# Optimization experiments

Hardware: AMD Instinct MI355X
Metric: run time of the kernel (lower is better)

## Reference

```python
import jax, jax.numpy as jnp
import numpy as np

B, T, V, E, H, L = 64, 512, 50000, 256, 256, 9


def _lstm_dir(x, w_ih, w_hh, b, reverse):
    # x: [B,T,I]; w_ih: [4H,I]; w_hh: [4H,H]; b: [4H]. PyTorch gate order i,f,g,o.
    Bm, Hm = x.shape[0], w_hh.shape[1]
    gx = jnp.einsum('bti,gi->btg', x, w_ih) + b  # [B,T,4H] precomputed input proj

    def step(carry, g_t):
        h, c = carry
        gates = g_t + h @ w_hh.T
        i, f, g, o = jnp.split(gates, 4, axis=-1)
        c = jax.nn.sigmoid(f) * c + jax.nn.sigmoid(i) * jnp.tanh(g)
        h = jax.nn.sigmoid(o) * jnp.tanh(c)
        return (h, c), h

    init = (jnp.zeros((Bm, Hm), x.dtype), jnp.zeros((Bm, Hm), x.dtype))
    _, hs = jax.lax.scan(step, init, jnp.swapaxes(gx, 0, 1), reverse=reverse)
    return jnp.swapaxes(hs, 0, 1)  # [B,T,H]


def _bilstm_layer(x, w_ih, w_hh, b):
    fwd = _lstm_dir(x, w_ih[0], w_hh[0], b[0], False)
    bwd = _lstm_dir(x, w_ih[1], w_hh[1], b[1], True)
    return jnp.concatenate([fwd, bwd], axis=-1)  # [B,T,2H]


def _crf_nll(emissions, labels, mask, trans, start_trans, end_trans):
    # emissions: [B,T,L]; labels: [B,T] int; mask: [B,T] (mask[:,0] assumed 1)
    maskf = mask.astype(emissions.dtype)
    # gold path score
    em_lab = jnp.take_along_axis(emissions, labels[..., None], axis=2)[..., 0]  # [B,T]
    trans_sc = trans[labels[:, :-1], labels[:, 1:]]  # [B,T-1]
    score = start_trans[labels[:, 0]] + em_lab[:, 0] \
        + jnp.sum((trans_sc + em_lab[:, 1:]) * maskf[:, 1:], axis=1)
    last_idx = jnp.sum(mask, axis=1).astype(jnp.int32) - 1
    last_lab = jnp.take_along_axis(labels, last_idx[:, None].astype(labels.dtype), axis=1)[:, 0]
    score = score + end_trans[last_lab]
    # log-partition via forward algorithm (scan over time)
    alpha0 = start_trans[None, :] + emissions[:, 0]  # [B,L]

    def step(alpha, xs):
        em_t, m_t = xs
        new = jax.nn.logsumexp(alpha[:, :, None] + trans[None], axis=1) + em_t
        alpha = jnp.where(m_t[:, None] > 0, new, alpha)
        return alpha, None

    alpha, _ = jax.lax.scan(
        step, alpha0,
        (jnp.swapaxes(emissions[:, 1:], 0, 1), jnp.swapaxes(mask[:, 1:], 0, 1)))
    logZ = jax.nn.logsumexp(alpha + end_trans[None, :], axis=1)  # [B]
    return -(score - logZ).mean()


def setup_inputs() -> dict:
    key = jax.random.key(0)
    ks = jax.random.split(key, 16)
    s = 0.05
    inp = {
        'input_ids': jax.random.randint(ks[0], (B, T), 0, V),
        'attention_mask': jnp.ones((B, T), jnp.int32),
        'labels': jax.random.randint(ks[1], (B, T), 0, L),
        'emb': jax.random.normal(ks[2], (V, E), jnp.float32) * s,
        # layer 0: input size E; layer 1: input size 2H. [dir, 4H, in]
        'w_ih0': jax.random.normal(ks[3], (2, 4 * H, E), jnp.float32) * s,
        'w_hh0': jax.random.normal(ks[4], (2, 4 * H, H), jnp.float32) * s,
        'b0': jax.random.normal(ks[5], (2, 4 * H), jnp.float32) * s,
        'w_ih1': jax.random.normal(ks[6], (2, 4 * H, 2 * H), jnp.float32) * s,
        'w_hh1': jax.random.normal(ks[7], (2, 4 * H, H), jnp.float32) * s,
        'b1': jax.random.normal(ks[8], (2, 4 * H), jnp.float32) * s,
        'lin_w': jax.random.normal(ks[9], (L, 2 * H), jnp.float32) * s,
        'lin_b': jax.random.normal(ks[10], (L,), jnp.float32) * s,
        'trans': jax.random.normal(ks[11], (L, L), jnp.float32) * 0.1,
        'start_trans': jax.random.normal(ks[12], (L,), jnp.float32) * 0.1,
        'end_trans': jax.random.normal(ks[13], (L,), jnp.float32) * 0.1,
    }
    return inp


def reference(input_ids, attention_mask, labels, emb, w_ih0, w_hh0, b0,
              w_ih1, w_hh1, b1, lin_w, lin_b, trans, start_trans, end_trans):
    x = emb[input_ids]                       # [B,T,E]
    x = _bilstm_layer(x, w_ih0, w_hh0, b0)   # [B,T,2H]
    x = _bilstm_layer(x, w_ih1, w_hh1, b1)   # [B,T,2H]
    emissions = x @ lin_w.T + lin_b          # [B,T,L]
    loss = _crf_nll(emissions, labels, attention_mask, trans, start_trans, end_trans)
    return loss
```

## Files before the change

### kernel.cpp

```cpp
#include <hip/hip_runtime.h>
#include <stdint.h>
#include <stddef.h>

#define B_ 64
#define T_ 512
#define E_ 256
#define H_ 256
#define L_ 9
#define BT (B_*T_)
#define G4 1024
#define N2 2048

typedef short    bf16x8  __attribute__((ext_vector_type(8)));
typedef float    f32x4   __attribute__((ext_vector_type(4)));
typedef int      i32x4   __attribute__((ext_vector_type(4)));
typedef int      i32x8   __attribute__((ext_vector_type(8)));

__device__ __forceinline__ unsigned short f2bf(float x){
    unsigned u = __builtin_bit_cast(unsigned, x);
    u += 0x7fffu + ((u >> 16) & 1u);
    return (unsigned short)(u >> 16);
}
__device__ __forceinline__ float bf2f(unsigned short h){
    unsigned u = ((unsigned)h) << 16;
    return __builtin_bit_cast(float, u);
}

__device__ __forceinline__ unsigned char f32_e4m3(float x){
    unsigned b = __builtin_bit_cast(unsigned, x);
    unsigned s = b >> 31;
    float a = fabsf(x);
    if (a >= 448.f) return (unsigned char)((s<<7) | 0x7E);
    int E = (int)((b>>23)&255) - 127;
    if (E < -6) E = -6;
    int qi = (int)rintf(a * exp2f((float)(3 - E)));
    if (qi >= 16){ qi >>= 1; ++E; }
    if (qi == 0) return (unsigned char)(s<<7);
    unsigned mag = (qi >= 8) ? ((((unsigned)(E + 7)) << 3) | (unsigned)(qi - 8))
                             : (unsigned)qi;
    return (unsigned char)((s<<7) | mag);
}

__device__ __forceinline__ float sigm(float x){
    return __builtin_amdgcn_rcpf(1.f + __expf(-x));
}
__device__ __forceinline__ float tanh_(float x){
    float e = __expf(2.f*x);
    return 1.f - 2.f*__builtin_amdgcn_rcpf(e + 1.f);
}

__device__ __forceinline__ void lds_load16(void* lds, const void* g){
    __builtin_amdgcn_global_load_lds(
        (const __attribute__((address_space(1))) void*)g,
        (__attribute__((address_space(3))) void*)lds, 16, 0, 0);
}

__device__ __forceinline__ void barrier_lds(){
    asm volatile("s_waitcnt lgkmcnt(0)" ::: "memory");
    __builtin_amdgcn_s_barrier();
    __builtin_amdgcn_sched_barrier(0);
}

__device__ __forceinline__ void store_out(unsigned short* p, float v){ *p = f2bf(v); }
__device__ __forceinline__ void store_out(float* p, float v){ *p = v; }

__global__ void k_embed(const int* __restrict__ ids, const float* __restrict__ emb,
                        unsigned char* __restrict__ x0){
    int bt = blockIdx.x;
    int e  = threadIdx.x;
    int id = ids[bt];
    x0[(size_t)bt*E_ + e] = f32_e4m3(emb[(size_t)id*E_ + e]);
}

__global__ void k_pack_wih(const float* __restrict__ in, unsigned char* __restrict__ out, int K){
    int p = blockIdx.y;
    int k = blockIdx.x*256 + threadIdx.x;
    int dirc = p >> 10, pp = p & 1023;
    int wv = pp >> 7, rem = pp & 127;
    int uh = (rem >> 6) & 1, g = (rem >> 4) & 3, ulx = rem & 15;
    int orig = dirc*1024 + g*256 + wv*32 + uh*16 + ulx;
    out[(size_t)p*K + k] = f32_e4m3(in[(size_t)orig*K + k]);
}

__global__ void k_pack_bias(const float* __restrict__ b, float* __restrict__ bp){
    int p = blockIdx.x*256 + threadIdx.x;
    int dirc = p >> 10, pp = p & 1023;
    int wv = pp >> 7, rem = pp & 127;
    int uh = (rem >> 6) & 1, g = (rem >> 4) & 3, ulx = rem & 15;
    int orig = dirc*1024 + g*256 + wv*32 + uh*16 + ulx;
    bp[p] = b[orig];
}

__global__ void k_pack_wfp8(const float* __restrict__ whh, unsigned char* __restrict__ wpk){
    int idx = blockIdx.x*256 + threadIdx.x;
    int lane = idx & 63;
    int uh   = (idx >> 6) & 1;
    int g    = (idx >> 7) & 3;
    int kt   = (idx >> 9) & 1;
    int wv   = (idx >> 10) & 7;
    int dir  = (idx >> 13) & 1;
    int ulx = lane & 15, hi4 = lane >> 4;
    int row = g*256 + wv*32 + uh*16 + ulx;
    int k0 = kt*128 + hi4*32;
    const float* src = whh + ((size_t)dir*G4 + row)*H_ + k0;
    unsigned char* dst = wpk + (size_t)idx*32;
    #pragma unroll
    for (int q = 0; q < 32; ++q) dst[q] = f32_e4m3(src[q]);
}

__global__ __launch_bounds__(256) void k_gemm_fp8(const unsigned char* __restrict__ A,
                                                  const unsigned char* __restrict__ Bm,
                                                  const float* __restrict__ bias,
                                                  unsigned short* __restrict__ C,
                                                  int M, int N, int K){
    __shared__ __align__(16) unsigned char As[16384];
    __shared__ __align__(16) unsigned char Bs[16384];
    int tid = threadIdx.x, lane = tid & 63, w = tid >> 6;
    int wm = w >> 1, wn = w & 1;
    int tileM = blockIdx.y * 128, tileN = blockIdx.x * 128;
    f32x4 acc[4][4] = {};
    for (int k0 = 0; k0 < K; k0 += 128){
        #pragma unroll
        for (int p = 0; p < 4; ++p){
            int idx = (p*256 + tid)*16;
            int ks = idx >> 12, rem = idx & 4095, row = rem >> 5;
            int jsrc = (rem & 16) ^ ((row & 4) << 2);
            lds_load16((char*)As + idx, A + (size_t)(tileM + row)*K + k0 + ks*32 + jsrc);
            lds_load16((char*)Bs + idx, Bm + (size_t)(tileN + row)*K + k0 + ks*32 + jsrc);
        }
        __syncthreads();
        int ks = lane >> 4, m15 = lane & 15;
        i32x8 af[4], bfv[4];
        #pragma unroll
        for (int mf = 0; mf < 4; ++mf){
            int r = wm*64 + mf*16 + m15;
            int base = ks*4096 + r*32, sw = (r & 4) << 2;
            i32x4 lo = *(const i32x4*)((const char*)As + base + sw);
            i32x4 hi = *(const i32x4*)((const char*)As + base + (16 ^ sw));
            af[mf] = __builtin_shufflevector(lo, hi, 0,1,2,3,4,5,6,7);
        }
        #pragma unroll
        for (int nf = 0; nf < 4; ++nf){
            int r = wn*64 + nf*16 + m15;
            int base = ks*4096 + r*32, sw = (r & 4) << 2;
            i32x4 lo = *(const i32x4*)((const char*)Bs + base + sw);
            i32x4 hi = *(const i32x4*)((const char*)Bs + base + (16 ^ sw));
            bfv[nf] = __builtin_shufflevector(lo, hi, 0,1,2,3,4,5,6,7);
        }
        #pragma unroll
        for (int mf = 0; mf < 4; ++mf)
            #pragma unroll
            for (int nf = 0; nf < 4; ++nf)
                acc[mf][nf] = __builtin_amdgcn_mfma_scale_f32_16x16x128_f8f6f4(
                                  af[mf], bfv[nf], acc[mf][nf],
                                  0, 0, 0, 0x7f7f7f7f, 0, 0x7f7f7f7f);
        barrier_lds();
    }
    #pragma unroll
    for (int mf = 0; mf < 4; ++mf){
        #pragma unroll
        for (int nf = 0; nf < 4; ++nf){
            int row0 = tileM + wm*64 + mf*16 + (lane >> 4)*4;
            int col  = tileN + wn*64 + nf*16 + (lane & 15);
            float bv = bias[col];
            #pragma unroll
            for (int r = 0; r < 4; ++r)
                C[(size_t)(row0 + r)*N + col] = f2bf(acc[mf][nf][r] + bv);
        }
    }
}

template<typename OutT>
__global__ __launch_bounds__(512, 2)
void k_rec_mfma(const unsigned short* __restrict__ gx,
                const unsigned char* __restrict__ wpk,
                OutT* __restrict__ out){
    int blk = blockIdx.x;
    int dir = blk & 1, bg = blk >> 1;
    int tid = threadIdx.x, lane = tid & 63, w = tid >> 6;
    int ul = lane & 15, hi4 = lane >> 4;
    int batch = bg*4 + hi4;

    __shared__ __align__(16) unsigned char hlds[2][32][16][8];
    {
        unsigned long long* hz = (unsigned long long*)hlds;
        for (int i = tid; i < 1024; i += 512) hz[i] = 0ull;
    }

    i32x8 wf[2][4][2];
    {
        const i32x8* wb = (const i32x8*)wpk;
        #pragma unroll
        for (int kt = 0; kt < 2; ++kt)
            #pragma unroll
            for (int g = 0; g < 4; ++g)
                #pragma unroll
                for (int uh = 0; uh < 2; ++uh)
                    wf[kt][g][uh] = wb[((((size_t)(dir*8 + w)*2 + kt)*4 + g)*2 + uh)*64 + lane];
    }
    __syncthreads();

    const unsigned short* gp = gx + (size_t)(batch*T_ + (dir ? T_-1 : 0))*N2
                                  + dir*1024 + w*128 + ul;
    ptrdiff_t dstep = dir ? -(ptrdiff_t)N2 : (ptrdiff_t)N2;

    unsigned short gxr[8];
    #pragma unroll
    for (int uh = 0; uh < 2; ++uh)
        #pragma unroll
        for (int g = 0; g < 4; ++g)
            gxr[uh*4+g] = gp[uh*64 + g*16];

    float c0 = 0.f, c1 = 0.f;
    int u0 = w*32 + ul, u1 = u0 + 16;
    OutT* ob = out + (size_t)batch*T_*512 + dir*256;

    for (int s = 0; s < T_; ++s){
        int buf = s & 1;
        f32x4 acc[4][2];
        #pragma unroll
        for (int g = 0; g < 4; ++g)
            #pragma unroll
            for (int uh = 0; uh < 2; ++uh)
                acc[g][uh] = (f32x4){ bf2f(gxr[uh*4+g]), 0.f, 0.f, 0.f };

        gp += dstep;
        unsigned short gxn[8];
        #pragma unroll
        for (int uh = 0; uh < 2; ++uh)
            #pragma unroll
            for (int g = 0; g < 4; ++g)
                gxn[uh*4+g] = gp[uh*64 + g*16];

        const unsigned long long* hrow = (const unsigned long long*)&hlds[buf][0][0][0];
        #pragma unroll
        for (int kt = 0; kt < 2; ++kt){
            unsigned long long a0 = hrow[(kt*16 + hi4*4 + 0)*16 + ul];
            unsigned long long a1 = hrow[(kt*16 + hi4*4 + 1)*16 + ul];
            unsigned long long a2 = hrow[(kt*16 + hi4*4 + 2)*16 + ul];
            unsigned long long a3 = hrow[(kt*16 + hi4*4 + 3)*16 + ul];
            i32x8 af = (i32x8){ (int)a0, (int)(a0>>32), (int)a1, (int)(a1>>32),
                                (int)a2, (int)(a2>>32), (int)a3, (int)(a3>>32) };
            #pragma unroll
            for (int g = 0; g < 4; ++g)
                #pragma unroll
                for (int uh = 0; uh < 2; ++uh)
                    acc[g][uh] = __builtin_amdgcn_mfma_scale_f32_16x16x128_f8f6f4(
                                     af, wf[kt][g][uh], acc[g][uh],
                                     0, 0, 0, 0x7f7f7f7f, 0, 0x7f7f7f7f);
        }

        int tt = dir ? (T_-1-s) : s;
        float h0, h1;
        {
            float xi = acc[0][0][0], xf = acc[1][0][0], xg = acc[2][0][0], xo = acc[3][0][0];
            c0 = sigm(xf)*c0 + sigm(xi)*tanh_(xg);
            h0 = sigm(xo)*tanh_(c0);
        }
        {
            float xi = acc[0][1][0], xf = acc[1][1][0], xg = acc[2][1][0], xo = acc[3][1][0];
            c1 = sigm(xf)*c1 + sigm(xi)*tanh_(xg);
            h1 = sigm(xo)*tanh_(c1);
        }

        unsigned char hb0, hb1;
#if __has_builtin(__builtin_amdgcn_cvt_pk_fp8_f32)
        {
            int pk = __builtin_amdgcn_cvt_pk_fp8_f32(h0, h1, 0, false);
            hb0 = (unsigned char)(pk & 0xff);
            hb1 = (unsigned char)((pk >> 8) & 0xff);
        }
#else
        hb0 = f32_e4m3(h0); hb1 = f32_e4m3(h1);
#endif
        hlds[buf^1][u0>>3][hi4*4][u0&7] = hb0;
        hlds[buf^1][u1>>3][hi4*4][u1&7] = hb1;

        if constexpr (sizeof(OutT) == 1){
            ((unsigned char*)ob)[(size_t)tt*512 + u0] = hb0;
            ((unsigned char*)ob)[(size_t)tt*512 + u1] = hb1;
        } else {
            store_out(&ob[(size_t)tt*512 + u0], h0);
            store_out(&ob[(size_t)tt*512 + u1], h1);
        }

        #pragma unroll
        for (int i = 0; i < 8; ++i) gxr[i] = gxn[i];
        barrier_lds();
    }
}

__global__ __launch_bounds__(256) void k_linear(const float* __restrict__ x,
                                                const float* __restrict__ w,
                                                const float* __restrict__ bias,
                                                float* __restrict__ em){
    int wv = threadIdx.x >> 6, lane = threadIdx.x & 63;
    int bt = blockIdx.x*4 + wv;
    const float4* xp = (const float4*)(x + (size_t)bt*(2*H_) + lane*8);
    float4 xa = xp[0], xb = xp[1];
    #pragma unroll
    for (int l = 0; l < L_; ++l){
        const float4* wp = (const float4*)(w + (size_t)l*(2*H_) + lane*8);
        float4 wa = wp[0], wb = wp[1];
        float p = xa.x*wa.x + xa.y*wa.y + xa.z*wa.z + xa.w*wa.w
                + xb.x*wb.x + xb.y*wb.y + xb.z*wb.z + xb.w*wb.w;
        #pragma unroll
        for (int o = 32; o; o >>= 1) p += __shfl_xor(p, o);
        if (lane == 0) em[(size_t)bt*L_ + l] = p + bias[l];
    }
}

__global__ void k_crf(const float* __restrict__ em, const int* __restrict__ labels,
                      const int* __restrict__ mask, const float* __restrict__ trans,
                      const float* __restrict__ st, const float* __restrict__ et,
                      float* __restrict__ out){
    int b = blockIdx.x, lane = threadIdx.x;
    __shared__ float tr[L_*L_];
    for (int i = lane; i < L_*L_; i += 64) tr[i] = trans[i];
    __syncthreads();
    const float* e  = em + (size_t)b*T_*L_;
    const int* lab  = labels + b*T_;
    const int* mk   = mask + b*T_;
    float sc = 0.f; int msum = 0;
    for (int t = lane; t < T_; t += 64){
        msum += mk[t];
        if (t >= 1)
            sc += (tr[lab[t-1]*L_ + lab[t]] + e[t*L_ + lab[t]]) * (float)mk[t];
    }
    #pragma unroll
    for (int o = 32; o; o >>= 1){ sc += __shfl_xor(sc, o); msum += __shfl_xor(msum, o); }
    int lj = lane < L_ ? lane : 0;
    float alpha = (lane < L_) ? (st[lj] + e[lj]) : -3.0e38f;
    for (int t = 1; t < T_; ++t){
        float v[L_]; float m = -3.0e38f;
        #pragma unroll
        for (int i = 0; i < L_; ++i){
            float ai = __shfl(alpha, i);
            v[i] = ai + tr[i*L_ + lj];
            m = fmaxf(m, v[i]);
        }
        float ssum = 0.f;
        #pragma unroll
        for (int i = 0; i < L_; ++i) ssum += __expf(v[i] - m);
        float nw = m + __logf(ssum) + e[t*L_ + lj];
        if (lane < L_ && mk[t] > 0) alpha = nw;
    }
    float av = (lane < L_) ? alpha + et[lj] : -3.0e38f;
    float m2 = av;
    #pragma unroll
    for (int o = 32; o; o >>= 1) m2 = fmaxf(m2, __shfl_xor(m2, o));
    float s2 = (lane < L_) ? __expf(av - m2) : 0.f;
    #pragma unroll
    for (int o = 32; o; o >>= 1) s2 += __shfl_xor(s2, o);
    if (lane == 0){
        float logZ = m2 + __logf(s2);
        int last = msum - 1;
        float score = sc + st[lab[0]] + e[lab[0]] + et[lab[last]];
        atomicAdd(out, (logZ - score) * (1.f/(float)B_));
    }
}

extern "C" void kernel_launch(void* const* d_in, const int* in_sizes, int n_in,
                              void* d_out, int out_size, void* d_ws, size_t ws_size,
                              hipStream_t stream){
    (void)in_sizes; (void)n_in; (void)out_size; (void)ws_size;
    const int*   ids    = (const int*)d_in[0];
    const int*   amask  = (const int*)d_in[1];
    const int*   labels = (const int*)d_in[2];
    const float* emb    = (const float*)d_in[3];
    const float* w_ih0  = (const float*)d_in[4];
    const float* w_hh0  = (const float*)d_in[5];
    const float* b0     = (const float*)d_in[6];
    const float* w_ih1  = (const float*)d_in[7];
    const float* w_hh1  = (const float*)d_in[8];
    const float* b1     = (const float*)d_in[9];
    const float* lin_w  = (const float*)d_in[10];
    const float* lin_b  = (const float*)d_in[11];
    const float* trans  = (const float*)d_in[12];
    const float* st     = (const float*)d_in[13];
    const float* et     = (const float*)d_in[14];
    float* out = (float*)d_out;

    char* ws = (char*)d_ws;
    size_t o = 0;
    auto alloc = [&](size_t bytes)->char*{
        char* p = ws + o; o = (o + bytes + 255) & ~(size_t)255; return p;
    };
    unsigned char*  x0    = (unsigned char*)alloc((size_t)BT*E_);
    unsigned char*  wih0p = (unsigned char*)alloc((size_t)N2*E_);
    unsigned char*  wih1p = (unsigned char*)alloc((size_t)N2*512);
    unsigned char*  wpk0  = (unsigned char*)alloc(16384*32);
    unsigned char*  wpk1  = (unsigned char*)alloc(16384*32);
    float*          bp0   = (float*)alloc(N2*4);
    float*          bp1   = (float*)alloc(N2*4);
    unsigned short* gx    = (unsigned short*)alloc((size_t)BT*N2*2);
    unsigned char*  xc1   = (unsigned char*)alloc((size_t)BT*512);
    float*          xc2   = (float*)alloc((size_t)BT*512*4);
    float*          em    = (float*)alloc((size_t)BT*L_*4 + 1024);

    hipMemsetAsync(d_out, 0, sizeof(float), stream);

    k_pack_wih<<<dim3(E_/256, N2), 256, 0, stream>>>(w_ih0, wih0p, E_);
    k_pack_wih<<<dim3(512/256, N2), 256, 0, stream>>>(w_ih1, wih1p, 512);
    k_pack_bias<<<N2/256, 256, 0, stream>>>(b0, bp0);
    k_pack_bias<<<N2/256, 256, 0, stream>>>(b1, bp1);
    k_pack_wfp8<<<16384/256, 256, 0, stream>>>(w_hh0, wpk0);
    k_pack_wfp8<<<16384/256, 256, 0, stream>>>(w_hh1, wpk1);
    k_embed<<<BT, E_, 0, stream>>>(ids, emb, x0);

    k_gemm_fp8<<<dim3(N2/128, BT/128), 256, 0, stream>>>(x0, wih0p, bp0, gx, BT, N2, E_);
    k_rec_mfma<unsigned char><<<32, 512, 0, stream>>>(gx, wpk0, xc1);
    k_gemm_fp8<<<dim3(N2/128, BT/128), 256, 0, stream>>>(xc1, wih1p, bp1, gx, BT, N2, 512);
    k_rec_mfma<float><<<32, 512, 0, stream>>>(gx, wpk1, xc2);

    k_linear<<<BT/4, 256, 0, stream>>>(xc2, lin_w, lin_b, em);
    k_crf<<<B_, 64, 0, stream>>>(em, labels, amask, trans, st, et, out);
}
```

Before: 1.317 ms.

## Double-buffer GEMM, vectorize recurrence gate loads, split MFMA chains, bf16 second-layer output

```diff
diff --git a/kernel.cpp b/kernel.cpp
--- a/kernel.cpp
+++ b/kernel.cpp
@@ -15,6 +15,7 @@
 typedef float    f32x4   __attribute__((ext_vector_type(4)));
 typedef int      i32x4   __attribute__((ext_vector_type(4)));
 typedef int      i32x8   __attribute__((ext_vector_type(8)));
+typedef unsigned short u16x8 __attribute__((ext_vector_type(8)));
 
 __device__ __forceinline__ unsigned short f2bf(float x){
     unsigned u = __builtin_bit_cast(unsigned, x);
@@ -49,6 +50,14 @@
     return 1.f - 2.f*__builtin_amdgcn_rcpf(e + 1.f);
 }
 
+__device__ __forceinline__ unsigned char f32_fp8(float x){
+#if __has_builtin(__builtin_amdgcn_cvt_pk_fp8_f32)
+    return (unsigned char)(__builtin_amdgcn_cvt_pk_fp8_f32(x, x, 0, false) & 0xff);
+#else
+    return f32_e4m3(x);
+#endif
+}
+
 __device__ __forceinline__ void lds_load16(void* lds, const void* g){
     __builtin_amdgcn_global_load_lds(
         (const __attribute__((address_space(1))) void*)g,
@@ -60,9 +69,6 @@
     __builtin_amdgcn_s_barrier();
     __builtin_amdgcn_sched_barrier(0);
 }
-
-__device__ __forceinline__ void store_out(unsigned short* p, float v){ *p = f2bf(v); }
-__device__ __forceinline__ void store_out(float* p, float v){ *p = v; }
 
 __global__ void k_embed(const int* __restrict__ ids, const float* __restrict__ emb,
                         unsigned char* __restrict__ x0){
@@ -77,7 +83,7 @@
     int k = blockIdx.x*256 + threadIdx.x;
     int dirc = p >> 10, pp = p & 1023;
     int wv = pp >> 7, rem = pp & 127;
-    int uh = (rem >> 6) & 1, g = (rem >> 4) & 3, ulx = rem & 15;
+    int ulx = rem >> 3, uh = (rem >> 2) & 1, g = rem & 3;
     int orig = dirc*1024 + g*256 + wv*32 + uh*16 + ulx;
     out[(size_t)p*K + k] = f32_e4m3(in[(size_t)orig*K + k]);
 }
@@ -86,7 +92,7 @@
     int p = blockIdx.x*256 + threadIdx.x;
     int dirc = p >> 10, pp = p & 1023;
     int wv = pp >> 7, rem = pp & 127;
-    int uh = (rem >> 6) & 1, g = (rem >> 4) & 3, ulx = rem & 15;
+    int ulx = rem >> 3, uh = (rem >> 2) & 1, g = rem & 3;
     int orig = dirc*1024 + g*256 + wv*32 + uh*16 + ulx;
     bp[p] = b[orig];
 }
@@ -113,38 +119,48 @@
                                                   const float* __restrict__ bias,
                                                   unsigned short* __restrict__ C,
                                                   int M, int N, int K){
-    __shared__ __align__(16) unsigned char As[16384];
-    __shared__ __align__(16) unsigned char Bs[16384];
+    __shared__ __align__(16) unsigned char As[2][16384];
+    __shared__ __align__(16) unsigned char Bs[2][16384];
     int tid = threadIdx.x, lane = tid & 63, w = tid >> 6;
     int wm = w >> 1, wn = w & 1;
-    int tileM = blockIdx.y * 128, tileN = blockIdx.x * 128;
-    f32x4 acc[4][4] = {};
-    for (int k0 = 0; k0 < K; k0 += 128){
+    int nwg = gridDim.x, qch = nwg >> 3;
+    int nid = (blockIdx.x & 7)*qch + (blockIdx.x >> 3);
+    int tileM = (nid >> 4) * 128, tileN = (nid & 15) * 128;
+    int nC = K >> 7;
+
+    auto stage = [&](int c, int buf){
         #pragma unroll
         for (int p = 0; p < 4; ++p){
             int idx = (p*256 + tid)*16;
             int ks = idx >> 12, rem = idx & 4095, row = rem >> 5;
             int jsrc = (rem & 16) ^ ((row & 4) << 2);
-            lds_load16((char*)As + idx, A + (size_t)(tileM + row)*K + k0 + ks*32 + jsrc);
-            lds_load16((char*)Bs + idx, Bm + (size_t)(tileN + row)*K + k0 + ks*32 + jsrc);
+            lds_load16(&As[buf][idx], A + (size_t)(tileM + row)*K + c*128 + ks*32 + jsrc);
+            lds_load16(&Bs[buf][idx], Bm + (size_t)(tileN + row)*K + c*128 + ks*32 + jsrc);
         }
-        __syncthreads();
+    };
+
+    stage(0, 0);
+    __syncthreads();
+    f32x4 acc[4][4] = {};
+    for (int c = 0; c < nC; ++c){
+        int buf = c & 1;
+        if (c + 1 < nC) stage(c + 1, buf ^ 1);
         int ks = lane >> 4, m15 = lane & 15;
         i32x8 af[4], bfv[4];
         #pragma unroll
         for (int mf = 0; mf < 4; ++mf){
             int r = wm*64 + mf*16 + m15;
             int base = ks*4096 + r*32, sw = (r & 4) << 2;
-            i32x4 lo = *(const i32x4*)((const char*)As + base + sw);
-            i32x4 hi = *(const i32x4*)((const char*)As + base + (16 ^ sw));
+            i32x4 lo = *(const i32x4*)(&As[buf][base + sw]);
+            i32x4 hi = *(const i32x4*)(&As[buf][base + (16 ^ sw)]);
             af[mf] = __builtin_shufflevector(lo, hi, 0,1,2,3,4,5,6,7);
         }
         #pragma unroll
         for (int nf = 0; nf < 4; ++nf){
             int r = wn*64 + nf*16 + m15;
             int base = ks*4096 + r*32, sw = (r & 4) << 2;
-            i32x4 lo = *(const i32x4*)((const char*)Bs + base + sw);
-            i32x4 hi = *(const i32x4*)((const char*)Bs + base + (16 ^ sw));
+            i32x4 lo = *(const i32x4*)(&Bs[buf][base + sw]);
+            i32x4 hi = *(const i32x4*)(&Bs[buf][base + (16 ^ sw)]);
             bfv[nf] = __builtin_shufflevector(lo, hi, 0,1,2,3,4,5,6,7);
         }
         #pragma unroll
@@ -154,7 +170,7 @@
                 acc[mf][nf] = __builtin_amdgcn_mfma_scale_f32_16x16x128_f8f6f4(
                                   af[mf], bfv[nf], acc[mf][nf],
                                   0, 0, 0, 0x7f7f7f7f, 0, 0x7f7f7f7f);
-        barrier_lds();
+        __syncthreads();
     }
     #pragma unroll
     for (int mf = 0; mf < 4; ++mf){
@@ -201,109 +217,112 @@
     __syncthreads();
 
     const unsigned short* gp = gx + (size_t)(batch*T_ + (dir ? T_-1 : 0))*N2
-                                  + dir*1024 + w*128 + ul;
+                                  + dir*1024 + w*128 + ul*8;
     ptrdiff_t dstep = dir ? -(ptrdiff_t)N2 : (ptrdiff_t)N2;
 
-    unsigned short gxr[8];
-    #pragma unroll
-    for (int uh = 0; uh < 2; ++uh)
-        #pragma unroll
-        for (int g = 0; g < 4; ++g)
-            gxr[uh*4+g] = gp[uh*64 + g*16];
-
+    u16x8 gxr = *(const u16x8*)gp;
     float c0 = 0.f, c1 = 0.f;
     int u0 = w*32 + ul, u1 = u0 + 16;
     OutT* ob = out + (size_t)batch*T_*512 + dir*256;
 
-    for (int s = 0; s < T_; ++s){
-        int buf = s & 1;
-        f32x4 acc[4][2];
-        #pragma unroll
-        for (int g = 0; g < 4; ++g)
-            #pragma unroll
-            for (int uh = 0; uh < 2; ++uh)
-                acc[g][uh] = (f32x4){ bf2f(gxr[uh*4+g]), 0.f, 0.f, 0.f };
-
-        gp += dstep;
-        unsigned short gxn[8];
-        #pragma unroll
-        for (int uh = 0; uh < 2; ++uh)
-            #pragma unroll
-            for (int g = 0; g < 4; ++g)
-                gxn[uh*4+g] = gp[uh*64 + g*16];
-
-        const unsigned long long* hrow = (const unsigned long long*)&hlds[buf][0][0][0];
-        #pragma unroll
-        for (int kt = 0; kt < 2; ++kt){
-            unsigned long long a0 = hrow[(kt*16 + hi4*4 + 0)*16 + ul];
-            unsigned long long a1 = hrow[(kt*16 + hi4*4 + 1)*16 + ul];
-            unsigned long long a2 = hrow[(kt*16 + hi4*4 + 2)*16 + ul];
-            unsigned long long a3 = hrow[(kt*16 + hi4*4 + 3)*16 + ul];
-            i32x8 af = (i32x8){ (int)a0, (int)(a0>>32), (int)a1, (int)(a1>>32),
-                                (int)a2, (int)(a2>>32), (int)a3, (int)(a3>>32) };
-            #pragma unroll
-            for (int g = 0; g < 4; ++g)
-                #pragma unroll
-                for (int uh = 0; uh < 2; ++uh)
-                    acc[g][uh] = __builtin_amdgcn_mfma_scale_f32_16x16x128_f8f6f4(
-                                     af, wf[kt][g][uh], acc[g][uh],
-                                     0, 0, 0, 0x7f7f7f7f, 0, 0x7f7f7f7f);
-        }
-
-        int tt = dir ? (T_-1-s) : s;
-        float h0, h1;
-        {
-            float xi = acc[0][0][0], xf = acc[1][0][0], xg = acc[2][0][0], xo = acc[3][0][0];
-            c0 = sigm(xf)*c0 + sigm(xi)*tanh_(xg);
-            h0 = sigm(xo)*tanh_(c0);
-        }
-        {
-            float xi = acc[0][1][0], xf = acc[1][1][0], xg = acc[2][1][0], xo = acc[3][1][0];
-            c1 = sigm(xf)*c1 + sigm(xi)*tanh_(xg);
-            h1 = sigm(xo)*tanh_(c1);
-        }
-
-        unsigned char hb0, hb1;
-#if __has_builtin(__builtin_amdgcn_cvt_pk_fp8_f32)
-        {
-            int pk = __builtin_amdgcn_cvt_pk_fp8_f32(h0, h1, 0, false);
-            hb0 = (unsigned char)(pk & 0xff);
-            hb1 = (unsigned char)((pk >> 8) & 0xff);
-        }
-#else
-        hb0 = f32_e4m3(h0); hb1 = f32_e4m3(h1);
-#endif
-        hlds[buf^1][u0>>3][hi4*4][u0&7] = hb0;
-        hlds[buf^1][u1>>3][hi4*4][u1&7] = hb1;
-
-        if constexpr (sizeof(OutT) == 1){
-            ((unsigned char*)ob)[(size_t)tt*512 + u0] = hb0;
-            ((unsigned char*)ob)[(size_t)tt*512 + u1] = hb1;
-        } else {
-            store_out(&ob[(size_t)tt*512 + u0], h0);
-            store_out(&ob[(size_t)tt*512 + u1], h1);
-        }
-
-        #pragma unroll
-        for (int i = 0; i < 8; ++i) gxr[i] = gxn[i];
-        barrier_lds();
-    }
-}
-
-__global__ __launch_bounds__(256) void k_linear(const float* __restrict__ x,
+#define REC_STEP(SV, BUF)                                                          \
+    {                                                                              \
+        const unsigned long long* hrow = (const unsigned long long*)&hlds[BUF][0][0][0]; \
+        unsigned long long a00 = hrow[(hi4*4 + 0)*16 + ul];                        \
+        unsigned long long a01 = hrow[(hi4*4 + 1)*16 + ul];                        \
+        unsigned long long a02 = hrow[(hi4*4 + 2)*16 + ul];                        \
+        unsigned long long a03 = hrow[(hi4*4 + 3)*16 + ul];                        \
+        unsigned long long a10 = hrow[(16 + hi4*4 + 0)*16 + ul];                   \
+        unsigned long long a11 = hrow[(16 + hi4*4 + 1)*16 + ul];                   \
+        unsigned long long a12 = hrow[(16 + hi4*4 + 2)*16 + ul];                   \
+        unsigned long long a13 = hrow[(16 + hi4*4 + 3)*16 + ul];                   \
+        i32x8 af0 = (i32x8){ (int)a00, (int)(a00>>32), (int)a01, (int)(a01>>32),   \
+                             (int)a02, (int)(a02>>32), (int)a03, (int)(a03>>32) }; \
+        i32x8 af1 = (i32x8){ (int)a10, (int)(a10>>32), (int)a11, (int)(a11>>32),   \
+                             (int)a12, (int)(a12>>32), (int)a13, (int)(a13>>32) }; \
+        gp += dstep;                                                               \
+        u16x8 gxn = *(const u16x8*)gp;                                             \
+        f32x4 acc0[4], acc1[4];                                                    \
+        _Pragma("unroll")                                                          \
+        for (int g = 0; g < 4; ++g){                                               \
+            acc0[g] = (f32x4){ bf2f(gxr[g]),   0.f, 0.f, 0.f };                    \
+            acc1[g] = (f32x4){ bf2f(gxr[4+g]), 0.f, 0.f, 0.f };                    \
+        }                                                                          \
+                                                          \
+        __builtin_amdgcn_s_setprio(1);                                             \
+        _Pragma("unroll")                                                          \
+        for (int g = 0; g < 4; ++g)                                                \
+            acc0[g] = __builtin_amdgcn_mfma_scale_f32_16x16x128_f8f6f4(            \
+                          af0, wf[0][g][0], acc0[g], 0, 0, 0, 0x7f7f7f7f, 0, 0x7f7f7f7f); \
+        _Pragma("unroll")                                                          \
+        for (int g = 0; g < 4; ++g)                                                \
+            acc0[g] = __builtin_amdgcn_mfma_scale_f32_16x16x128_f8f6f4(            \
+                          af1, wf[1][g][0], acc0[g], 0, 0, 0, 0x7f7f7f7f, 0, 0x7f7f7f7f); \
+        __builtin_amdgcn_s_setprio(0);                                             \
+                                           \
+        float h0;                                                                  \
+        {                                                                          \
+            float xi = acc0[0][0], xf = acc0[1][0], xg = acc0[2][0], xo = acc0[3][0]; \
+            c0 = sigm(xf)*c0 + sigm(xi)*tanh_(xg);                                 \
+            h0 = sigm(xo)*tanh_(c0);                                               \
+        }                                                                          \
+        unsigned char hb0 = f32_fp8(h0);                                           \
+        hlds[BUF^1][u0>>3][hi4*4][u0&7] = hb0;                                     \
+                                                          \
+        __builtin_amdgcn_s_setprio(1);                                             \
+        _Pragma("unroll")                                                          \
+        for (int g = 0; g < 4; ++g)                                                \
+            acc1[g] = __builtin_amdgcn_mfma_scale_f32_16x16x128_f8f6f4(            \
+                          af0, wf[0][g][1], acc1[g], 0, 0, 0, 0x7f7f7f7f, 0, 0x7f7f7f7f); \
+        _Pragma("unroll")                                                          \
+        for (int g = 0; g < 4; ++g)                                                \
+            acc1[g] = __builtin_amdgcn_mfma_scale_f32_16x16x128_f8f6f4(            \
+                          af1, wf[1][g][1], acc1[g], 0, 0, 0, 0x7f7f7f7f, 0, 0x7f7f7f7f); \
+        __builtin_amdgcn_s_setprio(0);                                             \
+        float h1;                                                                  \
+        {                                                                          \
+            float xi = acc1[0][0], xf = acc1[1][0], xg = acc1[2][0], xo = acc1[3][0]; \
+            c1 = sigm(xf)*c1 + sigm(xi)*tanh_(xg);                                 \
+            h1 = sigm(xo)*tanh_(c1);                                               \
+        }                                                                          \
+        unsigned char hb1 = f32_fp8(h1);                                           \
+        hlds[BUF^1][u1>>3][hi4*4][u1&7] = hb1;                                     \
+        barrier_lds();                                                             \
+                       \
+        int tt = dir ? (T_-1-(SV)) : (SV);                                         \
+        if constexpr (sizeof(OutT) == 1){                                          \
+            ((unsigned char*)ob)[(size_t)tt*512 + u0] = hb0;                       \
+            ((unsigned char*)ob)[(size_t)tt*512 + u1] = hb1;                       \
+        } else {                                                                   \
+            ob[(size_t)tt*512 + u0] = (OutT)f2bf(h0);                              \
+            ob[(size_t)tt*512 + u1] = (OutT)f2bf(h1);                              \
+        }                                                                          \
+        gxr = gxn;                                                                 \
+    }
+
+    for (int s = 0; s < T_; s += 2){
+        REC_STEP(s, 0)
+        REC_STEP(s+1, 1)
+    }
+#undef REC_STEP
+}
+
+__global__ __launch_bounds__(256) void k_linear(const unsigned short* __restrict__ x,
                                                 const float* __restrict__ w,
                                                 const float* __restrict__ bias,
                                                 float* __restrict__ em){
     int wv = threadIdx.x >> 6, lane = threadIdx.x & 63;
     int bt = blockIdx.x*4 + wv;
-    const float4* xp = (const float4*)(x + (size_t)bt*(2*H_) + lane*8);
-    float4 xa = xp[0], xb = xp[1];
+    u16x8 xv = *(const u16x8*)(x + (size_t)bt*(2*H_) + lane*8);
+    float xf[8];
+    #pragma unroll
+    for (int j = 0; j < 8; ++j) xf[j] = bf2f(xv[j]);
     #pragma unroll
     for (int l = 0; l < L_; ++l){
         const float4* wp = (const float4*)(w + (size_t)l*(2*H_) + lane*8);
         float4 wa = wp[0], wb = wp[1];
-        float p = xa.x*wa.x + xa.y*wa.y + xa.z*wa.z + xa.w*wa.w
-                + xb.x*wb.x + xb.y*wb.y + xb.z*wb.z + xb.w*wb.w;
+        float p = xf[0]*wa.x + xf[1]*wa.y + xf[2]*wa.z + xf[3]*wa.w
+                + xf[4]*wb.x + xf[5]*wb.y + xf[6]*wb.z + xf[7]*wb.w;
         #pragma unroll
         for (int o = 32; o; o >>= 1) p += __shfl_xor(p, o);
         if (lane == 0) em[(size_t)bt*L_ + l] = p + bias[l];
@@ -395,7 +414,7 @@
     float*          bp1   = (float*)alloc(N2*4);
     unsigned short* gx    = (unsigned short*)alloc((size_t)BT*N2*2);
     unsigned char*  xc1   = (unsigned char*)alloc((size_t)BT*512);
-    float*          xc2   = (float*)alloc((size_t)BT*512*4);
+    unsigned short* xc2   = (unsigned short*)alloc((size_t)BT*512*2);
     float*          em    = (float*)alloc((size_t)BT*L_*4 + 1024);
 
     hipMemsetAsync(d_out, 0, sizeof(float), stream);
@@ -408,10 +427,10 @@
     k_pack_wfp8<<<16384/256, 256, 0, stream>>>(w_hh1, wpk1);
     k_embed<<<BT, E_, 0, stream>>>(ids, emb, x0);
 
-    k_gemm_fp8<<<dim3(N2/128, BT/128), 256, 0, stream>>>(x0, wih0p, bp0, gx, BT, N2, E_);
+    k_gemm_fp8<<<4096, 256, 0, stream>>>(x0, wih0p, bp0, gx, BT, N2, E_);
     k_rec_mfma<unsigned char><<<32, 512, 0, stream>>>(gx, wpk0, xc1);
-    k_gemm_fp8<<<dim3(N2/128, BT/128), 256, 0, stream>>>(xc1, wih1p, bp1, gx, BT, N2, 512);
-    k_rec_mfma<float><<<32, 512, 0, stream>>>(gx, wpk1, xc2);
+    k_gemm_fp8<<<4096, 256, 0, stream>>>(xc1, wih1p, bp1, gx, BT, N2, 512);
+    k_rec_mfma<unsigned short><<<32, 512, 0, stream>>>(gx, wpk1, xc2);
 
     k_linear<<<BT/4, 256, 0, stream>>>(xc2, lin_w, lin_b, em);
     k_crf<<<B_, 64, 0, stream>>>(em, labels, amask, trans, st, et, out);
```

Measured after the change: 1.408 ms. 6.9% more time.
